# Optimization experiments

Hardware: AMD Instinct MI355X
Metric: run time of the kernel (lower is better)

## Reference

```python
import jax, jax.numpy as jnp
import numpy as np

D_MODEL = 1024
N_HEADS = 16
HEAD_DIM = D_MODEL // N_HEADS
ROPE_BASE = 10000.0


def setup_inputs() -> dict:
    key = jax.random.key(0)
    ks = jax.random.split(key, 5)
    B, S = 1, 4096
    scale = 1.0 / np.sqrt(D_MODEL)
    x = jax.random.normal(ks[0], (B, S, D_MODEL), dtype=jnp.float32)
    Wq = jax.random.normal(ks[1], (D_MODEL, D_MODEL), dtype=jnp.float32) * scale
    Wk = jax.random.normal(ks[2], (D_MODEL, D_MODEL), dtype=jnp.float32) * scale
    Wv = jax.random.normal(ks[3], (D_MODEL, D_MODEL), dtype=jnp.float32) * scale
    Wo = jax.random.normal(ks[4], (D_MODEL, D_MODEL), dtype=jnp.float32) * scale
    return {"x": x, "Wq": Wq, "Wk": Wk, "Wv": Wv, "Wo": Wo}


def _rope(q, k):
    # q, k: [B, S, H, Dh]
    S, Dh = q.shape[1], q.shape[-1]
    inv_freq = 1.0 / (ROPE_BASE ** (jnp.arange(0, Dh, 2, dtype=jnp.float32) / Dh))
    t = jnp.arange(S, dtype=jnp.float32)
    freqs = jnp.outer(t, inv_freq)                      # [S, Dh/2]
    emb = jnp.concatenate([freqs, freqs], axis=-1)      # [S, Dh]
    cos = jnp.cos(emb)[None, :, None, :]                # [1, S, 1, Dh]
    sin = jnp.sin(emb)[None, :, None, :]

    def rotate_half(v):
        v1, v2 = v[..., : Dh // 2], v[..., Dh // 2 :]
        return jnp.concatenate([-v2, v1], axis=-1)

    return q * cos + rotate_half(q) * sin, k * cos + rotate_half(k) * sin


def reference(x, Wq, Wk, Wv, Wo):
    B, S, _ = x.shape
    H, Dh = N_HEADS, HEAD_DIM
    # torch Linear: y = x @ W.T
    q = (x @ Wq.T).reshape(B, S, H, Dh)
    k = (x @ Wk.T).reshape(B, S, H, Dh)
    v = (x @ Wv.T).reshape(B, S, H, Dh)
    q, k = _rope(q, k)
    scale = 1.0 / np.sqrt(Dh)
    # scores: [B, H, S, S]
    scores = jnp.einsum("bqhd,bkhd->bhqk", q, k) * scale
    causal = jnp.triu(jnp.ones((S, S), dtype=bool), k=1)
    scores = jnp.where(causal, -jnp.inf, scores)
    attn = jax.nn.softmax(scores, axis=-1)
    out = jnp.einsum("bhqk,bkhd->bqhd", attn, v).reshape(B, S, H * Dh)
    return out @ Wo.T
```

## Files before the change

kernel.cpp:

```cpp
#include <hip/hip_runtime.h>
#include <hip/hip_bf16.h>

typedef __attribute__((ext_vector_type(8))) short bf16x8;
typedef __attribute__((ext_vector_type(4))) float f32x4;
typedef unsigned short u16;

#define S_LEN 4096
#define DM 1024
#define NH 16
#define DH 64

__device__ __forceinline__ u16 f2b_rne(float f) {
  unsigned u = __builtin_bit_cast(unsigned, f);
  return (u16)((u + 0x7fffu + ((u >> 16) & 1u)) >> 16);
}
__device__ __forceinline__ unsigned pk2(float a, float b) {
  unsigned ua = __builtin_bit_cast(unsigned, a);
  unsigned ub = __builtin_bit_cast(unsigned, b);
  ua = (ua + 0x7fffu + ((ua >> 16) & 1u)) >> 16;
  ub = (ub + 0x7fffu + ((ub >> 16) & 1u)) & 0xffff0000u;
  return ua | ub;
}
__device__ __forceinline__ unsigned pk2t(float a, float b) {
  return __builtin_amdgcn_perm(__builtin_bit_cast(unsigned, b),
                               __builtin_bit_cast(unsigned, a), 0x07060302u);
}

__device__ __forceinline__ void glds16(const u16* g, u16* l) {
  __builtin_amdgcn_global_load_lds(
      (const __attribute__((address_space(1))) unsigned int*)g,
      (__attribute__((address_space(3))) unsigned int*)l, 16, 0, 0);
}

__global__ __launch_bounds__(256) void cvt_all(const float* __restrict__ x,
                                               const float* __restrict__ Wq,
                                               const float* __restrict__ Wk,
                                               const float* __restrict__ Wv,
                                               const float* __restrict__ Wo,
                                               u16* __restrict__ xb, u16* __restrict__ wqb,
                                               u16* __restrict__ wkb, u16* __restrict__ wvb,
                                               u16* __restrict__ wob) {
  int idx = (blockIdx.x * 256 + threadIdx.x) * 4;
  const float* src;
  u16* dst;
  int o;
  if (idx < 4194304) {
    src = x; dst = xb; o = idx;
  } else {
    int t = idx - 4194304;
    int wsel = t >> 20;
    o = t & 1048575;
    src = (wsel == 0) ? Wq : (wsel == 1) ? Wk : (wsel == 2) ? Wv : Wo;
    dst = (wsel == 0) ? wqb : (wsel == 1) ? wkb : (wsel == 2) ? wvb : wob;
  }
  float4 v = *(const float4*)(src + o);
  uint2 ov;
  ov.x = pk2(v.x, v.y);
  ov.y = pk2(v.z, v.w);
  *(uint2*)(dst + o) = ov;
}

__global__ __launch_bounds__(256) void zero_kernel(float4* __restrict__ p) {
  p[blockIdx.x * 256 + threadIdx.x] = float4{0.f, 0.f, 0.f, 0.f};
}

__global__ __launch_bounds__(256) void qkv_gemm(const u16* __restrict__ A,
                                                const u16* __restrict__ Wq,
                                                const u16* __restrict__ Wk,
                                                const u16* __restrict__ Wv,
                                                u16* __restrict__ Qo, u16* __restrict__ Ko,
                                                u16* __restrict__ Vt) {
  __shared__ __align__(16) u16 As[2 * 128 * 32];
  __shared__ __align__(16) u16 Bs[2 * 128 * 32];
  const int mat = blockIdx.x >> 3;
  const u16* B = (mat == 0) ? Wq : (mat == 1) ? Wk : Wv;
  const int K = DM, N = DM;
  const int tid = threadIdx.x;
  const int wave = tid >> 6, lane = tid & 63;
  const int fm = lane & 15, fq = lane >> 4;
  const int mb = blockIdx.y * 128, nb = (blockIdx.x & 7) * 128;
  const int wm = (wave & 1) * 64, wn = (wave >> 1) * 64;

  f32x4 acc[4][4];
#pragma unroll
  for (int i = 0; i < 4; ++i)
#pragma unroll
    for (int j = 0; j < 4; ++j)
#pragma unroll
      for (int r = 0; r < 4; ++r) acc[i][j][r] = 0.f;

  const int r_ = tid >> 2;
  const int cg = (tid & 3) ^ ((r_ >> 1) & 3);
  const u16* Ag0 = A + (size_t)(mb + r_) * K + cg * 8;
  const u16* Ag1 = A + (size_t)(mb + r_ + 64) * K + cg * 8;
  const u16* Bg0 = B + (size_t)(nb + r_) * K + cg * 8;
  const u16* Bg1 = B + (size_t)(nb + r_ + 64) * K + cg * 8;
  const int l0 = wave * 512;
  const int l1 = 2048 + wave * 512;
  const int sw = (fm >> 1) & 3;

  int buf = 0;
  glds16(Ag0, As + l0);
  glds16(Ag1, As + l1);
  glds16(Bg0, Bs + l0);
  glds16(Bg1, Bs + l1);

  for (int k0 = 0; k0 < K; k0 += 32) {
    __syncthreads();
    if (k0 + 32 < K) {
      int bo = (buf ^ 1) * 4096;
      glds16(Ag0 + k0 + 32, As + bo + l0);
      glds16(Ag1 + k0 + 32, As + bo + l1);
      glds16(Bg0 + k0 + 32, Bs + bo + l0);
      glds16(Bg1 + k0 + 32, Bs + bo + l1);
    }
    const u16* Ab = As + buf * 4096;
    const u16* Bb = Bs + buf * 4096;
    bf16x8 av[4], bv[4];
#pragma unroll
    for (int t = 0; t < 4; ++t) {
      av[t] = *(const bf16x8*)(Ab + (wm + t * 16 + fm) * 32 + ((fq ^ sw) * 8));
      bv[t] = *(const bf16x8*)(Bb + (wn + t * 16 + fm) * 32 + ((fq ^ sw) * 8));
    }
#pragma unroll
    for (int i = 0; i < 4; ++i)
#pragma unroll
      for (int j = 0; j < 4; ++j)
        acc[i][j] = __builtin_amdgcn_mfma_f32_16x16x32_bf16(av[i], bv[j], acc[i][j], 0, 0, 0);
    buf ^= 1;
  }

  if (mat < 2) {
    u16* Out = (mat == 0) ? Qo : Ko;
    const float qs = (mat == 0) ? 0.1803368801111204f : 1.0f;
    const float c1 = -9.2103403719761836f / 32.f;
    const float if0 = __expf((float)fm * c1);
    const float if1 = __expf((float)(16 + fm) * c1);
#pragma unroll
    for (int ii = 0; ii < 4; ++ii) {
#pragma unroll
      for (int r = 0; r < 4; ++r) {
        float s = (float)(mb + wm + ii * 16 + fq * 4 + r);
#pragma unroll
        for (int jp = 0; jp < 2; ++jp) {
          float ang = s * (jp ? if1 : if0);
          float sn, cs;
          __sincosf(ang, &sn, &cs);
          float a = acc[ii][jp][r], b = acc[ii][jp + 2][r];
          acc[ii][jp][r] = (a * cs - b * sn) * qs;
          acc[ii][jp + 2][r] = (b * cs + a * sn) * qs;
        }
      }
    }
#pragma unroll
    for (int i = 0; i < 4; ++i)
#pragma unroll
      for (int j = 0; j < 4; ++j)
#pragma unroll
        for (int r = 0; r < 4; ++r) {
          int row = mb + wm + i * 16 + fq * 4 + r;
          int col = nb + wn + j * 16 + fm;
          Out[(size_t)row * N + col] = f2b_rne(acc[i][j][r]);
        }
  } else {
#pragma unroll
    for (int i = 0; i < 4; ++i)
#pragma unroll
      for (int j = 0; j < 4; ++j) {
        int col = nb + wn + j * 16 + fm;
        int row0 = mb + wm + i * 16 + fq * 4;
        uint2 pv;
        pv.x = pk2(acc[i][j][0], acc[i][j][1]);
        pv.y = pk2(acc[i][j][2], acc[i][j][3]);
        *(uint2*)(Vt + (size_t)col * S_LEN + row0) = pv;
      }
  }
}

__global__ __launch_bounds__(256) void o_gemm(const u16* __restrict__ A,
                                              const u16* __restrict__ B,
                                              float* __restrict__ C, int M, int N, int K) {
  __shared__ __align__(16) u16 As[2 * 64 * 32];
  __shared__ __align__(16) u16 Bs[2 * 128 * 32];
  const int tid = threadIdx.x;
  const int wave = tid >> 6, lane = tid & 63;
  const int fm = lane & 15, fq = lane >> 4;
  const int mb = blockIdx.y * 64, nb = blockIdx.x * 128;
  const int wm = (wave & 1) * 32, wn = (wave >> 1) * 64;

  f32x4 acc[2][4];
#pragma unroll
  for (int i = 0; i < 2; ++i)
#pragma unroll
    for (int j = 0; j < 4; ++j)
#pragma unroll
      for (int r = 0; r < 4; ++r) acc[i][j][r] = 0.f;

  const int r_ = tid >> 2;
  const int cg = (tid & 3) ^ ((r_ >> 1) & 3);
  const u16* Ag0 = A + (size_t)(mb + r_) * K + cg * 8;
  const u16* Bg0 = B + (size_t)(nb + r_) * K + cg * 8;
  const u16* Bg1 = B + (size_t)(nb + r_ + 64) * K + cg * 8;
  const int l0 = wave * 512;
  const int l1 = 2048 + wave * 512;
  const int sw = (fm >> 1) & 3;

  int buf = 0;
  glds16(Ag0, As + l0);
  glds16(Bg0, Bs + l0);
  glds16(Bg1, Bs + l1);

  for (int k0 = 0; k0 < K; k0 += 32) {
    __syncthreads();
    if (k0 + 32 < K) {
      int aoff = (buf ^ 1) * 2048, boff = (buf ^ 1) * 4096;
      glds16(Ag0 + k0 + 32, As + aoff + l0);
      glds16(Bg0 + k0 + 32, Bs + boff + l0);
      glds16(Bg1 + k0 + 32, Bs + boff + l1);
    }
    const u16* Ab = As + buf * 2048;
    const u16* Bb = Bs + buf * 4096;
    bf16x8 av[2], bv[4];
#pragma unroll
    for (int t = 0; t < 2; ++t)
      av[t] = *(const bf16x8*)(Ab + (wm + t * 16 + fm) * 32 + ((fq ^ sw) * 8));
#pragma unroll
    for (int t = 0; t < 4; ++t)
      bv[t] = *(const bf16x8*)(Bb + (wn + t * 16 + fm) * 32 + ((fq ^ sw) * 8));
#pragma unroll
    for (int i = 0; i < 2; ++i)
#pragma unroll
      for (int j = 0; j < 4; ++j)
        acc[i][j] = __builtin_amdgcn_mfma_f32_16x16x32_bf16(av[i], bv[j], acc[i][j], 0, 0, 0);
    buf ^= 1;
  }
#pragma unroll
  for (int i = 0; i < 2; ++i)
#pragma unroll
    for (int j = 0; j < 4; ++j)
#pragma unroll
      for (int r = 0; r < 4; ++r) {
        int row = mb + wm + i * 16 + fq * 4 + r;
        int col = nb + wn + j * 16 + fm;
        C[(size_t)row * N + col] = acc[i][j][r];
      }
}

template <int STORE>
__global__ __launch_bounds__(512, 4) void attn_kernel(const u16* __restrict__ Q,
                                                      const u16* __restrict__ K,
                                                      const u16* __restrict__ Vt,
                                                      float* __restrict__ Oacc,
                                                      float* __restrict__ Lacc) {
  __shared__ __align__(16) u16 Ks[2 * 4096];
  __shared__ __align__(16) u16 Vs[2 * 4096];
  const int tid = threadIdx.x;
  const int w = tid >> 6, lane = tid & 63;
  const int fm = lane & 15, fq = lane >> 4;
  const int bid = blockIdx.x;
  const int u = bid & 255, hi = bid >> 8;
  const int h = u & 15;
  const int qt0 = u >> 4;
  const int qt = hi ? qt0 : 15 - qt0;
  const int half = hi;
  const int qb = qt * 256 + w * 32;
  const int nlocal = 2 * qt + 2;
  const int kbase = half * nlocal;
  const int dtile = qb >> 6;

  bf16x8 q0[2], q1[2];
#pragma unroll
  for (int g = 0; g < 2; ++g) {
    const u16* qp = Q + (size_t)(qb + g * 16 + fm) * DM + h * DH + fq * 8;
    q0[g] = *(const bf16x8*)(qp);
    q1[g] = *(const bf16x8*)(qp + 32);
  }
  f32x4 o[2][4];
  f32x4 ls[2];
#pragma unroll
  for (int g = 0; g < 2; ++g) {
#pragma unroll
    for (int r = 0; r < 4; ++r) ls[g][r] = 0.f;
#pragma unroll
    for (int c4 = 0; c4 < 4; ++c4)
#pragma unroll
      for (int r = 0; r < 4; ++r) o[g][c4][r] = 0.f;
  }
  const short ONEB = (short)0x3F80;
  const bf16x8 vone = {ONEB, ONEB, ONEB, ONEB, ONEB, ONEB, ONEB, ONEB};

  const int rr = tid >> 3;
  const int cc8 = (tid & 7) ^ (rr & 7);
  const int grr = ((rr >> 5) << 5) | (((rr >> 2) & 3) << 3) | (((rr >> 4) & 1) << 2) | (rr & 3);
  const u16* Kg = K + (size_t)grr * DM + h * DH + cc8 * 8;
  const u16* Vg = Vt + (size_t)(h * DH + rr) * S_LEN + cc8 * 8;
  const int l0 = w * 512;
  const int sw7 = fm & 7;
  const f32x4 zf = {0.f, 0.f, 0.f, 0.f};

  glds16(Kg + (size_t)kbase * 64 * DM, Ks + l0);
  glds16(Vg + kbase * 64, Vs + l0);

  int buf = 0;
  for (int kl = 0; kl < nlocal; ++kl) {
    const int ktg = kbase + kl;
    __syncthreads();
    if (kl + 1 < nlocal) {
      int bo = (buf ^ 1) * 4096;
      glds16(Kg + (size_t)(ktg + 1) * 64 * DM, Ks + bo + l0);
      glds16(Vg + (ktg + 1) * 64, Vs + bo + l0);
    }
    if (ktg <= dtile) {
      const u16* Kb = Ks + buf * 4096;
      const u16* Vb = Vs + buf * 4096;

      f32x4 st[2][4];
#pragma unroll
      for (int t = 0; t < 4; ++t) {
        const u16* kr = Kb + (t * 16 + fm) * 64;
        bf16x8 ka = *(const bf16x8*)(kr + ((fq ^ sw7) * 8));
        bf16x8 kb2 = *(const bf16x8*)(kr + (((fq + 4) ^ sw7) * 8));
#pragma unroll
        for (int g = 0; g < 2; ++g) {
          f32x4 s = __builtin_amdgcn_mfma_f32_16x16x32_bf16(ka, q0[g], zf, 0, 0, 0);
          st[g][t] = __builtin_amdgcn_mfma_f32_16x16x32_bf16(kb2, q1[g], s, 0, 0, 0);
        }
      }
      if (ktg == dtile) {
#pragma unroll
        for (int g = 0; g < 2; ++g) {
          int qg = qb + g * 16 + fm;
#pragma unroll
          for (int t = 0; t < 4; ++t) {
            int key = ktg * 64 + (t >> 1) * 32 + fq * 8 + (t & 1) * 4;
#pragma unroll
            for (int r = 0; r < 4; ++r)
              st[g][t][r] = (key + r > qg) ? -1e30f : st[g][t][r];
          }
        }
      }
      bf16x8 pvb[4][2];
#pragma unroll
      for (int c4 = 0; c4 < 4; ++c4) {
        const u16* vr = Vb + (c4 * 16 + fm) * 64;
        pvb[c4][0] = *(const bf16x8*)(vr + ((fq ^ sw7) * 8));
        pvb[c4][1] = *(const bf16x8*)(vr + (((fq + 4) ^ sw7) * 8));
      }
#pragma unroll
      for (int g = 0; g < 2; ++g) {
        unsigned pw[8];
#pragma unroll
        for (int t = 0; t < 4; ++t) {
          float p0 = __builtin_amdgcn_exp2f(st[g][t][0]);
          float p1 = __builtin_amdgcn_exp2f(st[g][t][1]);
          float p2 = __builtin_amdgcn_exp2f(st[g][t][2]);
          float p3 = __builtin_amdgcn_exp2f(st[g][t][3]);
          pw[t * 2] = pk2t(p0, p1);
          pw[t * 2 + 1] = pk2t(p2, p3);
        }
        uint4 u0 = {pw[0], pw[1], pw[2], pw[3]};
        uint4 u1 = {pw[4], pw[5], pw[6], pw[7]};
        bf16x8 pb0 = __builtin_bit_cast(bf16x8, u0);
        bf16x8 pb1 = __builtin_bit_cast(bf16x8, u1);
        ls[g] = __builtin_amdgcn_mfma_f32_16x16x32_bf16(vone, pb0, ls[g], 0, 0, 0);
        ls[g] = __builtin_amdgcn_mfma_f32_16x16x32_bf16(vone, pb1, ls[g], 0, 0, 0);
#pragma unroll
        for (int c4 = 0; c4 < 4; ++c4) {
          o[g][c4] = __builtin_amdgcn_mfma_f32_16x16x32_bf16(pvb[c4][0], pb0, o[g][c4], 0, 0, 0);
          o[g][c4] = __builtin_amdgcn_mfma_f32_16x16x32_bf16(pvb[c4][1], pb1, o[g][c4], 0, 0, 0);
        }
      }
    }
    buf ^= 1;
  }
  if (STORE) {
    float* Ob = Oacc + (((size_t)half * NH + h) * S_LEN + qt * 256 + w * 32) * DH;
    float* Lb = Lacc + ((size_t)half * NH + h) * S_LEN + qt * 256 + w * 32;
#pragma unroll
    for (int g = 0; g < 2; ++g) {
      if (fq == 0) Lb[g * 16 + fm] = ls[g][0];
#pragma unroll
      for (int c4 = 0; c4 < 4; ++c4)
        *(float4*)(Ob + (size_t)(g * 16 + fm) * DH + c4 * 16 + fq * 4) =
            float4{o[g][c4][0], o[g][c4][1], o[g][c4][2], o[g][c4][3]};
    }
  } else {
    float* Ob = Oacc + ((size_t)h * S_LEN + qt * 256 + w * 32) * DH;
    float* Lb = Lacc + h * S_LEN + qt * 256 + w * 32;
#pragma unroll
    for (int g = 0; g < 2; ++g) {
      if (fq == 0) unsafeAtomicAdd(Lb + g * 16 + fm, ls[g][0]);
#pragma unroll
      for (int c4 = 0; c4 < 4; ++c4)
#pragma unroll
        for (int r = 0; r < 4; ++r)
          unsafeAtomicAdd(Ob + (size_t)(g * 16 + fm) * DH + c4 * 16 + fq * 4 + r, o[g][c4][r]);
    }
  }
}

__global__ __launch_bounds__(256) void combine2_kernel(const float* __restrict__ O0,
                                                       const float* __restrict__ O1,
                                                       const float* __restrict__ L0,
                                                       const float* __restrict__ L1,
                                                       u16* __restrict__ Ctx) {
  int idx = blockIdx.x * 256 + threadIdx.x;
  int d4 = (idx & 15) * 4;
  int hh = (idx >> 4) & 15;
  int row = idx >> 8;
  size_t ob = ((size_t)hh * S_LEN + row) * DH + d4;
  float4 a = *(const float4*)(O0 + ob);
  float4 b = *(const float4*)(O1 + ob);
  float il = 1.0f / (L0[hh * S_LEN + row] + L1[hh * S_LEN + row]);
  uint2 o;
  o.x = pk2((a.x + b.x) * il, (a.y + b.y) * il);
  o.y = pk2((a.z + b.z) * il, (a.w + b.w) * il);
  *(uint2*)(Ctx + (size_t)row * DM + hh * DH + d4) = o;
}

__global__ __launch_bounds__(256) void combine_kernel(const float* __restrict__ Oacc,
                                                      const float* __restrict__ Lacc,
                                                      u16* __restrict__ Ctx) {
  int idx = blockIdx.x * 256 + threadIdx.x;
  int d4 = (idx & 15) * 4;
  int hh = (idx >> 4) & 15;
  int row = idx >> 8;
  float4 a = *(const float4*)(Oacc + ((size_t)hh * S_LEN + row) * DH + d4);
  float il = 1.0f / Lacc[hh * S_LEN + row];
  uint2 o;
  o.x = pk2(a.x * il, a.y * il);
  o.y = pk2(a.z * il, a.w * il);
  *(uint2*)(Ctx + (size_t)row * DM + hh * DH + d4) = o;
}

extern "C" void kernel_launch(void* const* d_in, const int* in_sizes, int n_in,
                              void* d_out, int out_size, void* d_ws, size_t ws_size,
                              hipStream_t stream) {
  const float* x  = (const float*)d_in[0];
  const float* Wq = (const float*)d_in[1];
  const float* Wk = (const float*)d_in[2];
  const float* Wv = (const float*)d_in[3];
  const float* Wo = (const float*)d_in[4];
  float* out = (float*)d_out;

  const size_t MB = 1u << 20;
  char* ws = (char*)d_ws;

  if (ws_size >= 72 * MB) {
    u16* xb    = (u16*)(ws + 0 * MB);
    u16* wqb   = (u16*)(ws + 8 * MB);
    u16* wkb   = (u16*)(ws + 10 * MB);
    u16* wvb   = (u16*)(ws + 12 * MB);
    u16* wob   = (u16*)(ws + 14 * MB);
    u16* Qb    = (u16*)(ws + 16 * MB);
    u16* Kb    = (u16*)(ws + 24 * MB);
    u16* Vtb   = (u16*)(ws + 32 * MB);
    float* Op  = (float*)(ws + 40 * MB);
    float* Lp  = (float*)(ws + 8 * MB);
    u16* Ctx   = (u16*)(ws + 0 * MB);

    cvt_all<<<8192, 256, 0, stream>>>(x, Wq, Wk, Wv, Wo, xb, wqb, wkb, wvb, wob);
    qkv_gemm<<<dim3(24, 32), 256, 0, stream>>>(xb, wqb, wkb, wvb, Qb, Kb, Vtb);
    attn_kernel<1><<<512, 512, 0, stream>>>(Qb, Kb, Vtb, Op, Lp);
    combine2_kernel<<<4096, 256, 0, stream>>>(Op, Op + (size_t)NH * S_LEN * DH,
                                              Lp, Lp + (size_t)NH * S_LEN, Ctx);
    o_gemm<<<dim3(8, 64), 256, 0, stream>>>(Ctx, wob, out, S_LEN, DM, DM);
  } else {
    u16* xb    = (u16*)(ws + 0 * MB);
    u16* wqb   = (u16*)(ws + 8 * MB);
    u16* wkb   = (u16*)(ws + 10 * MB);
    u16* wvb   = (u16*)(ws + 12 * MB);
    float* Oacc = (float*)(ws + 0 * MB);
    float* Lacc = (float*)(ws + 16 * MB);
    u16* wob   = (u16*)(ws + 17 * MB);
    u16* Qb    = (u16*)(ws + 19 * MB);
    u16* Kb    = (u16*)(ws + 27 * MB);
    u16* Vtb   = (u16*)(ws + 35 * MB);
    u16* Ctx   = (u16*)(ws + 43 * MB);

    cvt_all<<<8192, 256, 0, stream>>>(x, Wq, Wk, Wv, Wo, xb, wqb, wkb, wvb, wob);
    qkv_gemm<<<dim3(24, 32), 256, 0, stream>>>(xb, wqb, wkb, wvb, Qb, Kb, Vtb);
    zero_kernel<<<4160, 256, 0, stream>>>((float4*)Oacc);
    attn_kernel<0><<<512, 512, 0, stream>>>(Qb, Kb, Vtb, Oacc, Lacc);
    combine_kernel<<<4096, 256, 0, stream>>>(Oacc, Lacc, Ctx);
    o_gemm<<<dim3(8, 64), 256, 0, stream>>>(Ctx, wob, out, S_LEN, DM, DM);
  }
}
```

Measured before the change: 199.3 us.

## Split attention key range four ways with a four-way combine kernel

Adds an NSPLIT template parameter to the attention kernel so each (query tile, head) can be split across four key-range partitions instead of two. This launches 1024 blocks rather than 512, to fill more of the GPU and shorten the per-block serial key loop. A new combine4 kernel sums the four partial outputs and normalisers. The price is more fp32 partial-output traffic and a larger workspace requirement, so the new path only runs when at least 104 MB of workspace is available.

```diff
diff --git a/kernel.cpp b/kernel.cpp
--- a/kernel.cpp
+++ b/kernel.cpp
@@ -246,7 +246,7 @@
       }
 }
 
-template <int STORE>
+template <int STORE, int NSPLIT>
 __global__ __launch_bounds__(512, 4) void attn_kernel(const u16* __restrict__ Q,
                                                       const u16* __restrict__ K,
                                                       const u16* __restrict__ Vt,
@@ -258,14 +258,23 @@
   const int w = tid >> 6, lane = tid & 63;
   const int fm = lane & 15, fq = lane >> 4;
   const int bid = blockIdx.x;
-  const int u = bid & 255, hi = bid >> 8;
-  const int h = u & 15;
-  const int qt0 = u >> 4;
-  const int qt = hi ? qt0 : 15 - qt0;
-  const int half = hi;
+  int qt, h, half, kbase, nlocal;
+  if (NSPLIT == 4) {
+    qt = 15 - (bid >> 6);
+    half = (bid >> 4) & 3;
+    h = bid & 15;
+    nlocal = qt + 1;
+    kbase = half * nlocal;
+  } else {
+    const int u = bid & 255, hi = bid >> 8;
+    h = u & 15;
+    const int qt0 = u >> 4;
+    qt = hi ? qt0 : 15 - qt0;
+    half = hi;
+    nlocal = 2 * qt + 2;
+    kbase = half * nlocal;
+  }
   const int qb = qt * 256 + w * 32;
-  const int nlocal = 2 * qt + 2;
-  const int kbase = half * nlocal;
   const int dtile = qb >> 6;
 
   bf16x8 q0[2], q1[2];
@@ -397,6 +406,27 @@
           unsafeAtomicAdd(Ob + (size_t)(g * 16 + fm) * DH + c4 * 16 + fq * 4 + r, o[g][c4][r]);
     }
   }
+}
+
+__global__ __launch_bounds__(256) void combine4_kernel(const float* __restrict__ O,
+                                                       const float* __restrict__ L,
+                                                       u16* __restrict__ Ctx) {
+  int idx = blockIdx.x * 256 + threadIdx.x;
+  int d4 = (idx & 15) * 4;
+  int hh = (idx >> 4) & 15;
+  int row = idx >> 8;
+  const size_t OS = (size_t)NH * S_LEN * DH, LS = (size_t)NH * S_LEN;
+  size_t ob = ((size_t)hh * S_LEN + row) * DH + d4;
+  size_t lb = (size_t)hh * S_LEN + row;
+  float4 a = *(const float4*)(O + ob);
+  float4 b = *(const float4*)(O + OS + ob);
+  float4 c = *(const float4*)(O + 2 * OS + ob);
+  float4 d = *(const float4*)(O + 3 * OS + ob);
+  float il = 1.0f / (L[lb] + L[LS + lb] + L[2 * LS + lb] + L[3 * LS + lb]);
+  uint2 o;
+  o.x = pk2((a.x + b.x + c.x + d.x) * il, (a.y + b.y + c.y + d.y) * il);
+  o.y = pk2((a.z + b.z + c.z + d.z) * il, (a.w + b.w + c.w + d.w) * il);
+  *(uint2*)(Ctx + (size_t)row * DM + hh * DH + d4) = o;
 }
 
 __global__ __launch_bounds__(256) void combine2_kernel(const float* __restrict__ O0,
@@ -446,7 +476,7 @@
   const size_t MB = 1u << 20;
   char* ws = (char*)d_ws;
 
-  if (ws_size >= 72 * MB) {
+  if (ws_size >= 104 * MB) {
     u16* xb    = (u16*)(ws + 0 * MB);
     u16* wqb   = (u16*)(ws + 8 * MB);
     u16* wkb   = (u16*)(ws + 10 * MB);
@@ -461,7 +491,25 @@
 
     cvt_all<<<8192, 256, 0, stream>>>(x, Wq, Wk, Wv, Wo, xb, wqb, wkb, wvb, wob);
     qkv_gemm<<<dim3(24, 32), 256, 0, stream>>>(xb, wqb, wkb, wvb, Qb, Kb, Vtb);
-    attn_kernel<1><<<512, 512, 0, stream>>>(Qb, Kb, Vtb, Op, Lp);
+    attn_kernel<1, 4><<<1024, 512, 0, stream>>>(Qb, Kb, Vtb, Op, Lp);
+    combine4_kernel<<<4096, 256, 0, stream>>>(Op, Lp, Ctx);
+    o_gemm<<<dim3(8, 64), 256, 0, stream>>>(Ctx, wob, out, S_LEN, DM, DM);
+  } else if (ws_size >= 72 * MB) {
+    u16* xb    = (u16*)(ws + 0 * MB);
+    u16* wqb   = (u16*)(ws + 8 * MB);
+    u16* wkb   = (u16*)(ws + 10 * MB);
+    u16* wvb   = (u16*)(ws + 12 * MB);
+    u16* wob   = (u16*)(ws + 14 * MB);
+    u16* Qb    = (u16*)(ws + 16 * MB);
+    u16* Kb    = (u16*)(ws + 24 * MB);
+    u16* Vtb   = (u16*)(ws + 32 * MB);
+    float* Op  = (float*)(ws + 40 * MB);
+    float* Lp  = (float*)(ws + 8 * MB);
+    u16* Ctx   = (u16*)(ws + 0 * MB);
+
+    cvt_all<<<8192, 256, 0, stream>>>(x, Wq, Wk, Wv, Wo, xb, wqb, wkb, wvb, wob);
+    qkv_gemm<<<dim3(24, 32), 256, 0, stream>>>(xb, wqb, wkb, wvb, Qb, Kb, Vtb);
+    attn_kernel<1, 2><<<512, 512, 0, stream>>>(Qb, Kb, Vtb, Op, Lp);
     combine2_kernel<<<4096, 256, 0, stream>>>(Op, Op + (size_t)NH * S_LEN * DH,
                                               Lp, Lp + (size_t)NH * S_LEN, Ctx);
     o_gemm<<<dim3(8, 64), 256, 0, stream>>>(Ctx, wob, out, S_LEN, DM, DM);
@@ -481,7 +529,7 @@
     cvt_all<<<8192, 256, 0, stream>>>(x, Wq, Wk, Wv, Wo, xb, wqb, wkb, wvb, wob);
     qkv_gemm<<<dim3(24, 32), 256, 0, stream>>>(xb, wqb, wkb, wvb, Qb, Kb, Vtb);
     zero_kernel<<<4160, 256, 0, stream>>>((float4*)Oacc);
-    attn_kernel<0><<<512, 512, 0, stream>>>(Qb, Kb, Vtb, Oacc, Lacc);
+    attn_kernel<0, 2><<<512, 512, 0, stream>>>(Qb, Kb, Vtb, Oacc, Lacc);
     combine_kernel<<<4096, 256, 0, stream>>>(Oacc, Lacc, Ctx);
     o_gemm<<<dim3(8, 64), 256, 0, stream>>>(Ctx, wob, out, S_LEN, DM, DM);
   }
```

New measurement: 198.2 us. Within noise of the previous version (-0.5%).

## Split attention KV range four ways with 4-wave blocks of 64 query rows each

Applied to the files above, without the earlier changes.

The attention kernel now uses 256-thread blocks where each wave handles 64 query rows instead of 32. This doubles Q reuse per K/V tile loaded into shared memory. The KV range is split into four partitions instead of two, giving 1024 blocks for better load balance. The partial outputs are stored as bf16 to cut write and read traffic, and a new combine4 kernel sums the four partials. The trade-offs are higher register pressure, a more complex causal mask condition, and some precision loss from storing bf16 partials.

```diff
diff --git a/kernel.cpp b/kernel.cpp
--- a/kernel.cpp
+++ b/kernel.cpp
@@ -24,6 +24,9 @@
 __device__ __forceinline__ unsigned pk2t(float a, float b) {
   return __builtin_amdgcn_perm(__builtin_bit_cast(unsigned, b),
                                __builtin_bit_cast(unsigned, a), 0x07060302u);
+}
+__device__ __forceinline__ float b2f(unsigned u) {
+  return __builtin_bit_cast(float, u << 16);
 }
 
 __device__ __forceinline__ void glds16(const u16* g, u16* l) {
@@ -246,39 +249,48 @@
       }
 }
 
-template <int STORE>
-__global__ __launch_bounds__(512, 4) void attn_kernel(const u16* __restrict__ Q,
-                                                      const u16* __restrict__ K,
-                                                      const u16* __restrict__ Vt,
-                                                      float* __restrict__ Oacc,
-                                                      float* __restrict__ Lacc) {
+template <int STORE, int NSPLIT>
+__global__ __launch_bounds__(256) void attn_kernel(const u16* __restrict__ Q,
+                                                   const u16* __restrict__ K,
+                                                   const u16* __restrict__ Vt,
+                                                   void* __restrict__ Oacc,
+                                                   float* __restrict__ Lacc) {
   __shared__ __align__(16) u16 Ks[2 * 4096];
   __shared__ __align__(16) u16 Vs[2 * 4096];
   const int tid = threadIdx.x;
   const int w = tid >> 6, lane = tid & 63;
   const int fm = lane & 15, fq = lane >> 4;
   const int bid = blockIdx.x;
-  const int u = bid & 255, hi = bid >> 8;
-  const int h = u & 15;
-  const int qt0 = u >> 4;
-  const int qt = hi ? qt0 : 15 - qt0;
-  const int half = hi;
-  const int qb = qt * 256 + w * 32;
-  const int nlocal = 2 * qt + 2;
-  const int kbase = half * nlocal;
-  const int dtile = qb >> 6;
-
-  bf16x8 q0[2], q1[2];
-#pragma unroll
-  for (int g = 0; g < 2; ++g) {
+  int qt, h, half, kbase, nlocal;
+  if (NSPLIT == 4) {
+    qt = 15 - (bid >> 6);
+    half = (bid >> 4) & 3;
+    h = bid & 15;
+    nlocal = qt + 1;
+    kbase = half * nlocal;
+  } else {
+    const int u = bid & 255, hi = bid >> 8;
+    h = u & 15;
+    const int qt0 = u >> 4;
+    qt = hi ? qt0 : 15 - qt0;
+    half = hi;
+    nlocal = 2 * qt + 2;
+    kbase = half * nlocal;
+  }
+  const int qb = qt * 256 + w * 64;
+  const int dtile = (qb + 63) >> 6;
+
+  bf16x8 q0[4], q1[4];
+#pragma unroll
+  for (int g = 0; g < 4; ++g) {
     const u16* qp = Q + (size_t)(qb + g * 16 + fm) * DM + h * DH + fq * 8;
     q0[g] = *(const bf16x8*)(qp);
     q1[g] = *(const bf16x8*)(qp + 32);
   }
-  f32x4 o[2][4];
-  f32x4 ls[2];
-#pragma unroll
-  for (int g = 0; g < 2; ++g) {
+  f32x4 o[4][4];
+  f32x4 ls[4];
+#pragma unroll
+  for (int g = 0; g < 4; ++g) {
 #pragma unroll
     for (int r = 0; r < 4; ++r) ls[g][r] = 0.f;
 #pragma unroll
@@ -291,15 +303,18 @@
 
   const int rr = tid >> 3;
   const int cc8 = (tid & 7) ^ (rr & 7);
-  const int grr = ((rr >> 5) << 5) | (((rr >> 2) & 3) << 3) | (((rr >> 4) & 1) << 2) | (rr & 3);
+  const int grr = (((rr >> 2) & 3) << 3) | (((rr >> 4) & 1) << 2) | (rr & 3);
   const u16* Kg = K + (size_t)grr * DM + h * DH + cc8 * 8;
   const u16* Vg = Vt + (size_t)(h * DH + rr) * S_LEN + cc8 * 8;
   const int l0 = w * 512;
+  const int l1 = 2048 + w * 512;
   const int sw7 = fm & 7;
   const f32x4 zf = {0.f, 0.f, 0.f, 0.f};
 
   glds16(Kg + (size_t)kbase * 64 * DM, Ks + l0);
+  glds16(Kg + (size_t)(kbase * 64 + 32) * DM, Ks + l1);
   glds16(Vg + kbase * 64, Vs + l0);
+  glds16(Vg + 32 * S_LEN + kbase * 64, Vs + l1);
 
   int buf = 0;
   for (int kl = 0; kl < nlocal; ++kl) {
@@ -307,28 +322,30 @@
     __syncthreads();
     if (kl + 1 < nlocal) {
       int bo = (buf ^ 1) * 4096;
-      glds16(Kg + (size_t)(ktg + 1) * 64 * DM, Ks + bo + l0);
+      glds16(Kg + (size_t)((ktg + 1) * 64) * DM, Ks + bo + l0);
+      glds16(Kg + (size_t)((ktg + 1) * 64 + 32) * DM, Ks + bo + l1);
       glds16(Vg + (ktg + 1) * 64, Vs + bo + l0);
+      glds16(Vg + 32 * S_LEN + (ktg + 1) * 64, Vs + bo + l1);
     }
     if (ktg <= dtile) {
       const u16* Kb = Ks + buf * 4096;
       const u16* Vb = Vs + buf * 4096;
 
-      f32x4 st[2][4];
+      f32x4 st[4][4];
 #pragma unroll
       for (int t = 0; t < 4; ++t) {
         const u16* kr = Kb + (t * 16 + fm) * 64;
         bf16x8 ka = *(const bf16x8*)(kr + ((fq ^ sw7) * 8));
         bf16x8 kb2 = *(const bf16x8*)(kr + (((fq + 4) ^ sw7) * 8));
 #pragma unroll
-        for (int g = 0; g < 2; ++g) {
+        for (int g = 0; g < 4; ++g) {
           f32x4 s = __builtin_amdgcn_mfma_f32_16x16x32_bf16(ka, q0[g], zf, 0, 0, 0);
           st[g][t] = __builtin_amdgcn_mfma_f32_16x16x32_bf16(kb2, q1[g], s, 0, 0, 0);
         }
       }
-      if (ktg == dtile) {
-#pragma unroll
-        for (int g = 0; g < 2; ++g) {
+      if (ktg >= (qb >> 6)) {
+#pragma unroll
+        for (int g = 0; g < 4; ++g) {
           int qg = qb + g * 16 + fm;
 #pragma unroll
           for (int t = 0; t < 4; ++t) {
@@ -347,7 +364,7 @@
         pvb[c4][1] = *(const bf16x8*)(vr + (((fq + 4) ^ sw7) * 8));
       }
 #pragma unroll
-      for (int g = 0; g < 2; ++g) {
+      for (int g = 0; g < 4; ++g) {
         unsigned pw[8];
 #pragma unroll
         for (int t = 0; t < 4; ++t) {
@@ -374,21 +391,24 @@
     buf ^= 1;
   }
   if (STORE) {
-    float* Ob = Oacc + (((size_t)half * NH + h) * S_LEN + qt * 256 + w * 32) * DH;
-    float* Lb = Lacc + ((size_t)half * NH + h) * S_LEN + qt * 256 + w * 32;
-#pragma unroll
-    for (int g = 0; g < 2; ++g) {
+    u16* Ob = (u16*)Oacc + (((size_t)half * NH + h) * S_LEN + qt * 256 + w * 64) * DH;
+    float* Lb = Lacc + ((size_t)half * NH + h) * S_LEN + qt * 256 + w * 64;
+#pragma unroll
+    for (int g = 0; g < 4; ++g) {
       if (fq == 0) Lb[g * 16 + fm] = ls[g][0];
 #pragma unroll
-      for (int c4 = 0; c4 < 4; ++c4)
-        *(float4*)(Ob + (size_t)(g * 16 + fm) * DH + c4 * 16 + fq * 4) =
-            float4{o[g][c4][0], o[g][c4][1], o[g][c4][2], o[g][c4][3]};
+      for (int c4 = 0; c4 < 4; ++c4) {
+        uint2 pv;
+        pv.x = pk2(o[g][c4][0], o[g][c4][1]);
+        pv.y = pk2(o[g][c4][2], o[g][c4][3]);
+        *(uint2*)(Ob + (size_t)(g * 16 + fm) * DH + c4 * 16 + fq * 4) = pv;
+      }
     }
   } else {
-    float* Ob = Oacc + ((size_t)h * S_LEN + qt * 256 + w * 32) * DH;
-    float* Lb = Lacc + h * S_LEN + qt * 256 + w * 32;
-#pragma unroll
-    for (int g = 0; g < 2; ++g) {
+    float* Ob = (float*)Oacc + ((size_t)h * S_LEN + qt * 256 + w * 64) * DH;
+    float* Lb = Lacc + h * S_LEN + qt * 256 + w * 64;
+#pragma unroll
+    for (int g = 0; g < 4; ++g) {
       if (fq == 0) unsafeAtomicAdd(Lb + g * 16 + fm, ls[g][0]);
 #pragma unroll
       for (int c4 = 0; c4 < 4; ++c4)
@@ -399,22 +419,29 @@
   }
 }
 
-__global__ __launch_bounds__(256) void combine2_kernel(const float* __restrict__ O0,
-                                                       const float* __restrict__ O1,
-                                                       const float* __restrict__ L0,
-                                                       const float* __restrict__ L1,
+__global__ __launch_bounds__(256) void combine4_kernel(const u16* __restrict__ O,
+                                                       const float* __restrict__ L,
                                                        u16* __restrict__ Ctx) {
   int idx = blockIdx.x * 256 + threadIdx.x;
   int d4 = (idx & 15) * 4;
   int hh = (idx >> 4) & 15;
   int row = idx >> 8;
+  const size_t OS = (size_t)NH * S_LEN * DH, LS = (size_t)NH * S_LEN;
   size_t ob = ((size_t)hh * S_LEN + row) * DH + d4;
-  float4 a = *(const float4*)(O0 + ob);
-  float4 b = *(const float4*)(O1 + ob);
-  float il = 1.0f / (L0[hh * S_LEN + row] + L1[hh * S_LEN + row]);
+  size_t lb = (size_t)hh * S_LEN + row;
+  float s0 = 0.f, s1 = 0.f, s2 = 0.f, s3 = 0.f;
+#pragma unroll
+  for (int s = 0; s < 4; ++s) {
+    uint2 v = *(const uint2*)(O + s * OS + ob);
+    s0 += b2f(v.x & 0xffffu);
+    s1 += b2f(v.x >> 16);
+    s2 += b2f(v.y & 0xffffu);
+    s3 += b2f(v.y >> 16);
+  }
+  float il = 1.0f / (L[lb] + L[LS + lb] + L[2 * LS + lb] + L[3 * LS + lb]);
   uint2 o;
-  o.x = pk2((a.x + b.x) * il, (a.y + b.y) * il);
-  o.y = pk2((a.z + b.z) * il, (a.w + b.w) * il);
+  o.x = pk2(s0 * il, s1 * il);
+  o.y = pk2(s2 * il, s3 * il);
   *(uint2*)(Ctx + (size_t)row * DM + hh * DH + d4) = o;
 }
 
@@ -455,15 +482,14 @@
     u16* Qb    = (u16*)(ws + 16 * MB);
     u16* Kb    = (u16*)(ws + 24 * MB);
     u16* Vtb   = (u16*)(ws + 32 * MB);
-    float* Op  = (float*)(ws + 40 * MB);
+    u16* Op    = (u16*)(ws + 40 * MB);
     float* Lp  = (float*)(ws + 8 * MB);
     u16* Ctx   = (u16*)(ws + 0 * MB);
 
     cvt_all<<<8192, 256, 0, stream>>>(x, Wq, Wk, Wv, Wo, xb, wqb, wkb, wvb, wob);
     qkv_gemm<<<dim3(24, 32), 256, 0, stream>>>(xb, wqb, wkb, wvb, Qb, Kb, Vtb);
-    attn_kernel<1><<<512, 512, 0, stream>>>(Qb, Kb, Vtb, Op, Lp);
-    combine2_kernel<<<4096, 256, 0, stream>>>(Op, Op + (size_t)NH * S_LEN * DH,
-                                              Lp, Lp + (size_t)NH * S_LEN, Ctx);
+    attn_kernel<1, 4><<<1024, 256, 0, stream>>>(Qb, Kb, Vtb, Op, Lp);
+    combine4_kernel<<<4096, 256, 0, stream>>>(Op, Lp, Ctx);
     o_gemm<<<dim3(8, 64), 256, 0, stream>>>(Ctx, wob, out, S_LEN, DM, DM);
   } else {
     u16* xb    = (u16*)(ws + 0 * MB);
@@ -481,7 +507,7 @@
     cvt_all<<<8192, 256, 0, stream>>>(x, Wq, Wk, Wv, Wo, xb, wqb, wkb, wvb, wob);
     qkv_gemm<<<dim3(24, 32), 256, 0, stream>>>(xb, wqb, wkb, wvb, Qb, Kb, Vtb);
     zero_kernel<<<4160, 256, 0, stream>>>((float4*)Oacc);
-    attn_kernel<0><<<512, 512, 0, stream>>>(Qb, Kb, Vtb, Oacc, Lacc);
+    attn_kernel<0, 2><<<512, 256, 0, stream>>>(Qb, Kb, Vtb, Oacc, Lacc);
     combine_kernel<<<4096, 256, 0, stream>>>(Oacc, Lacc, Ctx);
     o_gemm<<<dim3(8, 64), 256, 0, stream>>>(Ctx, wob, out, S_LEN, DM, DM);
   }
```

After: 214.9 us. 7.8% more time.
